# Kernel optimization log

Measured on AMD Instinct MI355X. Metric: run time of the kernel, lower is better.

## Reference

```python
import jax, jax.numpy as jnp
import numpy as np

K, NP, LAT = 400000, 8, 128
# Dense layer dims: (n_p+2) -> 128 -> 128 -> 128 -> 128 -> n_p -> n_p -> (n_p+2)
DIMS = [NP + 2, LAT, LAT, LAT, LAT, NP, NP, NP + 2]


def setup_inputs() -> dict:
    key = jax.random.key(0)
    ks = jax.random.split(key, 8)
    inp = {
        "data": jax.random.normal(ks[0], (K * NP,), dtype=jnp.float32),
        # element node ids: index * (n_p + 1), as assumed by updateElement
        "elements": jnp.arange(K, dtype=jnp.int32) * (NP + 1),
    }
    for i in range(7):
        inp[f"W{i}"] = jax.random.normal(ks[i + 1], (DIMS[i], DIMS[i + 1]), dtype=jnp.float32) / np.float32(np.sqrt(DIMS[i]))
        inp[f"b{i}"] = jnp.zeros((DIMS[i + 1],), dtype=jnp.float32)
    return inp


def _forward(data, elements, Ws, bs):
    k = elements.shape[0]
    n_p = data.size // k
    d2 = data.reshape(k, n_p)                      # (k, n_p)
    e = elements // (n_p + 1)                      # element indices 0..k-1
    left = (e - 1) % k                             # periodic left neighbor
    right = (e + 1) % k                            # periodic right neighbor
    # gather: [left elem last node, own n_p nodes, right elem first node]
    sent = jnp.concatenate(
        [d2[left, -1][:, None], d2[e], d2[right, 0][:, None]], axis=1
    )                                              # (k, n_p+2)
    # ResNetBlock: for each block size: Dense -> relu -> Dense; then final Dense; residual add
    f = sent
    for i in range(0, 6, 2):
        f = jax.nn.relu(f @ Ws[i] + bs[i])
        f = f @ Ws[i + 1] + bs[i + 1]
    f = f @ Ws[6] + bs[6]                          # (k, n_p+2)
    out = sent + f
    return out[:, 1:-1].reshape(-1)                # drop halo cols, flatten to (k*n_p,)


def reference(data, elements, W0, b0, W1, b1, W2, b2, W3, b3, W4, b4, W5, b5, W6, b6):
    Ws = [W0, W1, W2, W3, W4, W5, W6]
    bs = [b0, b1, b2, b3, b4, b5, b6]
    return _forward(data, elements, Ws, bs)
```

## Files before the change

kernel.cpp:

```cpp
#include <hip/hip_runtime.h>
#include <stdint.h>

#define KTOT 400000

typedef __attribute__((ext_vector_type(8))) short sh8;
typedef __attribute__((ext_vector_type(4))) float f32x4;

typedef sh8      __attribute__((may_alias)) sh8_a;
typedef uint64_t __attribute__((may_alias)) u64_a;
typedef uint4    __attribute__((may_alias)) uint4_a;
typedef float4   __attribute__((may_alias)) float4_a;

__device__ __forceinline__ ushort f2bf(float f){
  union { float f; uint32_t u; } v; v.f = f;
  return (ushort)((v.u + 0x7FFFu + ((v.u >> 16) & 1u)) >> 16);
}

__device__ __forceinline__ int actoff(int rt, int bi, int kbyte){
  return (((rt << 4) + bi) << 8) + (kbyte ^ ((bi & 7) << 4));
}

template<int KS, int NT, bool RELU>
__device__ __forceinline__ void layerf(const uint4* __restrict__ wf,
                                       const float* __restrict__ bp,
                                       char* actb, int lane)
{
  const int bi = lane & 15, g = lane >> 4;
  sh8 w[KS][NT];
  #pragma unroll
  for (int ks = 0; ks < KS; ks++)
    #pragma unroll
    for (int nt = 0; nt < NT; nt++)
      w[ks][nt] = __builtin_bit_cast(sh8, wf[(ks*NT + nt)*64 + lane]);

  float4 bv[NT];
  #pragma unroll
  for (int nt = 0; nt < NT; nt++)
    bv[nt] = *(const float4_a*)(bp + nt*16 + g*4);

  #pragma unroll
  for (int rt = 0; rt < 4; rt++){
    sh8 a[KS];
    #pragma unroll
    for (int ks = 0; ks < KS; ks++)
      a[ks] = *(const sh8_a*)(actb + actoff(rt, bi, ks*64 + g*16));

    f32x4 acc[NT];
    #pragma unroll
    for (int nt = 0; nt < NT; nt++)
      acc[nt] = (f32x4){bv[nt].x, bv[nt].y, bv[nt].z, bv[nt].w};

    #pragma unroll
    for (int ks = 0; ks < KS; ks++)
      #pragma unroll
      for (int nt = 0; nt < NT; nt++)
        acc[nt] = __builtin_amdgcn_mfma_f32_16x16x32_bf16(w[ks][nt], a[ks], acc[nt], 0, 0, 0);

    #pragma unroll
    for (int nt = 0; nt < NT; nt++){
      float x0 = acc[nt][0], x1 = acc[nt][1], x2 = acc[nt][2], x3 = acc[nt][3];
      if (RELU){ x0 = fmaxf(x0, 0.f); x1 = fmaxf(x1, 0.f);
                 x2 = fmaxf(x2, 0.f); x3 = fmaxf(x3, 0.f); }
      uint32_t lo = (uint32_t)f2bf(x0) | ((uint32_t)f2bf(x1) << 16);
      uint32_t hi = (uint32_t)f2bf(x2) | ((uint32_t)f2bf(x3) << 16);
      uint64_t pk = (uint64_t)lo | ((uint64_t)hi << 32);
      *(u64_a*)(actb + actoff(rt, bi, nt*32 + g*8)) = pk;
    }
  }
  __syncthreads();
}

__global__ __launch_bounds__(64, 2)
void gnn_kernel(const float* __restrict__ data, const int* __restrict__ elements,
                const uint4* __restrict__ wf, const float* __restrict__ bp,
                float* __restrict__ out)
{
  __shared__ uint4 actsm[1024];
  __shared__ __align__(16) float fbuf[256];
  char* actb = (char*)actsm;
  const int lane = threadIdx.x;
  const int r0 = blockIdx.x * 64;

  #pragma unroll
  for (int rt = 0; rt < 4; rt++){
    if (lane < 16){
      int row = r0 + (rt << 4) + lane;
      int e = elements[row] / 9;
      int le = (e == 0) ? KTOT - 1 : e - 1;
      int re = (e == KTOT - 1) ? 0 : e + 1;
      float lf = data[le*8 + 7];
      float4 d0 = *(const float4_a*)(data + e*8);
      float4 d1 = *(const float4_a*)(data + e*8 + 4);
      float rf = data[re*8];
      ushort s0=f2bf(lf),  s1=f2bf(d0.x), s2=f2bf(d0.y), s3=f2bf(d0.z), s4=f2bf(d0.w),
             s5=f2bf(d1.x), s6=f2bf(d1.y), s7=f2bf(d1.z), s8=f2bf(d1.w), s9=f2bf(rf);
      uint32_t p0 = s0 | ((uint32_t)s1 << 16), p1 = s2 | ((uint32_t)s3 << 16),
               p2 = s4 | ((uint32_t)s5 << 16), p3 = s6 | ((uint32_t)s7 << 16),
               p4 = s8 | ((uint32_t)s9 << 16);
      *(uint4_a*)(actb + actoff(rt, lane, 0 )) = make_uint4(p0, p1, p2, p3);
      *(uint4_a*)(actb + actoff(rt, lane, 16)) = make_uint4(p4, 0, 0, 0);
      *(uint4_a*)(actb + actoff(rt, lane, 32)) = make_uint4(0, 0, 0, 0);
      *(uint4_a*)(actb + actoff(rt, lane, 48)) = make_uint4(0, 0, 0, 0);
    }
  }
  __syncthreads();

  layerf<1, 8, true >(wf +   0*64, bp +   0, actb, lane);
  layerf<4, 8, false>(wf +   8*64, bp + 128, actb, lane);
  layerf<4, 8, true >(wf +  40*64, bp + 256, actb, lane);
  layerf<4, 8, false>(wf +  72*64, bp + 384, actb, lane);
  layerf<4, 1, true >(wf + 104*64, bp + 512, actb, lane);
  layerf<1, 1, false>(wf + 108*64, bp + 528, actb, lane);

  {
    const int bi = lane & 15, g = lane >> 4;
    sh8 w = __builtin_bit_cast(sh8, wf[109*64 + lane]);
    float4 bv = *(const float4_a*)(bp + 544 + g*4);
    #pragma unroll
    for (int rt = 0; rt < 4; rt++){
      sh8 a = *(const sh8_a*)(actb + actoff(rt, bi, g*16));
      f32x4 acc = (f32x4){bv.x, bv.y, bv.z, bv.w};
      acc = __builtin_amdgcn_mfma_f32_16x16x32_bf16(w, a, acc, 0, 0, 0);
      *(float4_a*)(&fbuf[bi*16 + g*4]) = make_float4(acc[0], acc[1], acc[2], acc[3]);
      __syncthreads();
      #pragma unroll
      for (int t = 0; t < 2; t++){
        int i = lane + t*64;
        int rr = i >> 3, c = i & 7;
        int row = r0 + (rt << 4) + rr;
        int e = elements[row] / 9;
        out[row*8 + c] = data[e*8 + c] + fbuf[rr*16 + c + 1];
      }
      __syncthreads();
    }
  }
}

__global__ void prep_kernel(const float* __restrict__ W0, const float* __restrict__ b0,
                            const float* __restrict__ W1, const float* __restrict__ b1,
                            const float* __restrict__ W2, const float* __restrict__ b2,
                            const float* __restrict__ W3, const float* __restrict__ b3,
                            const float* __restrict__ W4, const float* __restrict__ b4,
                            const float* __restrict__ W5, const float* __restrict__ b5,
                            const float* __restrict__ W6, const float* __restrict__ b6,
                            uint4* __restrict__ wsfrag, float* __restrict__ biaspad)
{
  int tid = blockIdx.x * 256 + threadIdx.x;
  if (tid < 110*64){
    int frag = tid >> 6, lane = tid & 63;
    const int off[8] = {0, 8, 40, 72, 104, 108, 109, 110};
    const int Kd[7]  = {10, 128, 128, 128, 128, 8, 8};
    const int Nd[7]  = {128, 128, 128, 128, 8, 8, 10};
    const int NTt[7] = {8, 8, 8, 8, 1, 1, 1};
    int l = 0;
    while (frag >= off[l+1]) l++;
    int local = frag - off[l];
    int nt = local % NTt[l];
    int ks = local / NTt[l];
    const float* W = (l==0)?W0:(l==1)?W1:(l==2)?W2:(l==3)?W3:(l==4)?W4:(l==5)?W5:W6;
    int K = Kd[l], N = Nd[l];
    int n = nt*16 + (lane & 15);
    int kbase = ks*32 + ((lane >> 4) << 3);
    ushort us[8];
    #pragma unroll
    for (int j = 0; j < 8; j++){
      int k = kbase + j;
      float v = (k < K && n < N) ? W[k*N + n] : 0.f;
      us[j] = f2bf(v);
    }
    uint32_t p0 = (uint32_t)us[0] | ((uint32_t)us[1] << 16);
    uint32_t p1 = (uint32_t)us[2] | ((uint32_t)us[3] << 16);
    uint32_t p2 = (uint32_t)us[4] | ((uint32_t)us[5] << 16);
    uint32_t p3 = (uint32_t)us[6] | ((uint32_t)us[7] << 16);
    wsfrag[frag*64 + lane] = make_uint4(p0, p1, p2, p3);
  } else if (tid < 110*64 + 560){
    int i = tid - 110*64;
    float v;
    if (i < 512){
      int l = i >> 7, idx = i & 127;
      const float* B = (l==0)?b0:(l==1)?b1:(l==2)?b2:b3;
      v = B[idx];
    } else {
      int j = i - 512;
      int l = j >> 4, idx = j & 15;
      const float* B = (l==0)?b4:(l==1)?b5:b6;
      int N = (l==2) ? 10 : 8;
      v = (idx < N) ? B[idx] : 0.f;
    }
    biaspad[i] = v;
  }
}

extern "C" void kernel_launch(void* const* d_in, const int* in_sizes, int n_in,
                              void* d_out, int out_size, void* d_ws, size_t ws_size,
                              hipStream_t stream)
{
  const float* data     = (const float*)d_in[0];
  const int*   elements = (const int*)  d_in[1];
  const float* W[7]; const float* B[7];
  for (int i = 0; i < 7; i++){ W[i] = (const float*)d_in[2 + 2*i]; B[i] = (const float*)d_in[3 + 2*i]; }

  uint4* wf = (uint4*)d_ws;
  float* bp = (float*)((char*)d_ws + 110*64*16);

  prep_kernel<<<30, 256, 0, stream>>>(W[0],B[0],W[1],B[1],W[2],B[2],W[3],B[3],
                                      W[4],B[4],W[5],B[5],W[6],B[6], wf, bp);
  gnn_kernel<<<KTOT/64, 64, 0, stream>>>(data, elements, wf, bp, (float*)d_out);
}
```

Before: 154.9 us.

## Fold the last two linear layers into one and parallelize the input gather

The final two dense layers have no activation between them, so W5·W6 and b5·W6+b6 are premultiplied in the prep kernel, removing one MFMA layer and one barrier from the main kernel. A zero pad is written after layer 4's outputs so the folded layer's K=32 MFMA reads zeros. The input gather now uses all 64 lanes, one row each, instead of 16 lanes looping over four row tiles. bf16 conversion switches to the HIP intrinsic. Folding changes rounding slightly because the intermediate bf16 step is gone.

```diff
diff --git a/kernel.cpp b/kernel.cpp
--- a/kernel.cpp
+++ b/kernel.cpp
@@ -1,4 +1,5 @@
 #include <hip/hip_runtime.h>
+#include <hip/hip_bf16.h>
 #include <stdint.h>
 
 #define KTOT 400000
@@ -7,20 +8,22 @@
 typedef __attribute__((ext_vector_type(4))) float f32x4;
 
 typedef sh8      __attribute__((may_alias)) sh8_a;
-typedef uint64_t __attribute__((may_alias)) u64_a;
+typedef uint2    __attribute__((may_alias)) uint2_a;
 typedef uint4    __attribute__((may_alias)) uint4_a;
 typedef float4   __attribute__((may_alias)) float4_a;
 
-__device__ __forceinline__ ushort f2bf(float f){
-  union { float f; uint32_t u; } v; v.f = f;
-  return (ushort)((v.u + 0x7FFFu + ((v.u >> 16) & 1u)) >> 16);
+__device__ __forceinline__ ushort f2bf16(float f){
+  return __builtin_bit_cast(ushort, __float2bfloat16(f));
+}
+__device__ __forceinline__ uint32_t pkbf(float lo, float hi){
+  return (uint32_t)f2bf16(lo) | ((uint32_t)f2bf16(hi) << 16);
 }
 
 __device__ __forceinline__ int actoff(int rt, int bi, int kbyte){
   return (((rt << 4) + bi) << 8) + (kbyte ^ ((bi & 7) << 4));
 }
 
-template<int KS, int NT, bool RELU>
+template<int KS, int NT, bool RELU, bool ZPAD>
 __device__ __forceinline__ void layerf(const uint4* __restrict__ wf,
                                        const float* __restrict__ bp,
                                        char* actb, int lane)
@@ -61,11 +64,11 @@
       float x0 = acc[nt][0], x1 = acc[nt][1], x2 = acc[nt][2], x3 = acc[nt][3];
       if (RELU){ x0 = fmaxf(x0, 0.f); x1 = fmaxf(x1, 0.f);
                  x2 = fmaxf(x2, 0.f); x3 = fmaxf(x3, 0.f); }
-      uint32_t lo = (uint32_t)f2bf(x0) | ((uint32_t)f2bf(x1) << 16);
-      uint32_t hi = (uint32_t)f2bf(x2) | ((uint32_t)f2bf(x3) << 16);
-      uint64_t pk = (uint64_t)lo | ((uint64_t)hi << 32);
-      *(u64_a*)(actb + actoff(rt, bi, nt*32 + g*8)) = pk;
-    }
+      uint32_t lo = pkbf(x0, x1), hi = pkbf(x2, x3);
+      *(uint2_a*)(actb + actoff(rt, bi, nt*32 + g*8)) = make_uint2(lo, hi);
+    }
+    if (ZPAD)
+      *(uint2_a*)(actb + actoff(rt, bi, 32 + g*8)) = make_uint2(0u, 0u);
   }
   __syncthreads();
 }
@@ -80,42 +83,36 @@
   char* actb = (char*)actsm;
   const int lane = threadIdx.x;
   const int r0 = blockIdx.x * 64;
-
-  #pragma unroll
-  for (int rt = 0; rt < 4; rt++){
-    if (lane < 16){
-      int row = r0 + (rt << 4) + lane;
-      int e = elements[row] / 9;
-      int le = (e == 0) ? KTOT - 1 : e - 1;
-      int re = (e == KTOT - 1) ? 0 : e + 1;
-      float lf = data[le*8 + 7];
-      float4 d0 = *(const float4_a*)(data + e*8);
-      float4 d1 = *(const float4_a*)(data + e*8 + 4);
-      float rf = data[re*8];
-      ushort s0=f2bf(lf),  s1=f2bf(d0.x), s2=f2bf(d0.y), s3=f2bf(d0.z), s4=f2bf(d0.w),
-             s5=f2bf(d1.x), s6=f2bf(d1.y), s7=f2bf(d1.z), s8=f2bf(d1.w), s9=f2bf(rf);
-      uint32_t p0 = s0 | ((uint32_t)s1 << 16), p1 = s2 | ((uint32_t)s3 << 16),
-               p2 = s4 | ((uint32_t)s5 << 16), p3 = s6 | ((uint32_t)s7 << 16),
-               p4 = s8 | ((uint32_t)s9 << 16);
-      *(uint4_a*)(actb + actoff(rt, lane, 0 )) = make_uint4(p0, p1, p2, p3);
-      *(uint4_a*)(actb + actoff(rt, lane, 16)) = make_uint4(p4, 0, 0, 0);
-      *(uint4_a*)(actb + actoff(rt, lane, 32)) = make_uint4(0, 0, 0, 0);
-      *(uint4_a*)(actb + actoff(rt, lane, 48)) = make_uint4(0, 0, 0, 0);
-    }
+  const int bi = lane & 15, g = lane >> 4;
+
+  {
+    int row = r0 + lane;
+    int e = elements[row] / 9;
+    int le = (e == 0) ? KTOT - 1 : e - 1;
+    int re = (e == KTOT - 1) ? 0 : e + 1;
+    float lf = data[le*8 + 7];
+    float4 d0 = *(const float4_a*)(data + e*8);
+    float4 d1 = *(const float4_a*)(data + e*8 + 4);
+    float rf = data[re*8];
+    uint32_t p0 = pkbf(lf,   d0.x), p1 = pkbf(d0.y, d0.z),
+             p2 = pkbf(d0.w, d1.x), p3 = pkbf(d1.y, d1.z),
+             p4 = pkbf(d1.w, rf);
+    *(uint4_a*)(actb + actoff(g, bi, 0 )) = make_uint4(p0, p1, p2, p3);
+    *(uint4_a*)(actb + actoff(g, bi, 16)) = make_uint4(p4, 0, 0, 0);
+    *(uint4_a*)(actb + actoff(g, bi, 32)) = make_uint4(0, 0, 0, 0);
+    *(uint4_a*)(actb + actoff(g, bi, 48)) = make_uint4(0, 0, 0, 0);
   }
   __syncthreads();
 
-  layerf<1, 8, true >(wf +   0*64, bp +   0, actb, lane);
-  layerf<4, 8, false>(wf +   8*64, bp + 128, actb, lane);
-  layerf<4, 8, true >(wf +  40*64, bp + 256, actb, lane);
-  layerf<4, 8, false>(wf +  72*64, bp + 384, actb, lane);
-  layerf<4, 1, true >(wf + 104*64, bp + 512, actb, lane);
-  layerf<1, 1, false>(wf + 108*64, bp + 528, actb, lane);
+  layerf<1, 8, true , false>(wf +   0*64, bp +   0, actb, lane);
+  layerf<4, 8, false, false>(wf +   8*64, bp + 128, actb, lane);
+  layerf<4, 8, true , false>(wf +  40*64, bp + 256, actb, lane);
+  layerf<4, 8, false, false>(wf +  72*64, bp + 384, actb, lane);
+  layerf<4, 1, true , true >(wf + 104*64, bp + 512, actb, lane);
 
   {
-    const int bi = lane & 15, g = lane >> 4;
-    sh8 w = __builtin_bit_cast(sh8, wf[109*64 + lane]);
-    float4 bv = *(const float4_a*)(bp + 544 + g*4);
+    sh8 w = __builtin_bit_cast(sh8, wf[108*64 + lane]);
+    float4 bv = *(const float4_a*)(bp + 528 + g*4);
     #pragma unroll
     for (int rt = 0; rt < 4; rt++){
       sh8 a = *(const sh8_a*)(actb + actoff(rt, bi, g*16));
@@ -146,18 +143,18 @@
                             uint4* __restrict__ wsfrag, float* __restrict__ biaspad)
 {
   int tid = blockIdx.x * 256 + threadIdx.x;
-  if (tid < 110*64){
+  if (tid < 109*64){
     int frag = tid >> 6, lane = tid & 63;
-    const int off[8] = {0, 8, 40, 72, 104, 108, 109, 110};
-    const int Kd[7]  = {10, 128, 128, 128, 128, 8, 8};
-    const int Nd[7]  = {128, 128, 128, 128, 8, 8, 10};
-    const int NTt[7] = {8, 8, 8, 8, 1, 1, 1};
+    const int off[7] = {0, 8, 40, 72, 104, 108, 109};
+    const int Kd[6]  = {10, 128, 128, 128, 128, 8};
+    const int Nd[6]  = {128, 128, 128, 128, 8, 10};
+    const int NTt[6] = {8, 8, 8, 8, 1, 1};
     int l = 0;
     while (frag >= off[l+1]) l++;
     int local = frag - off[l];
     int nt = local % NTt[l];
     int ks = local / NTt[l];
-    const float* W = (l==0)?W0:(l==1)?W1:(l==2)?W2:(l==3)?W3:(l==4)?W4:(l==5)?W5:W6;
+    const float* W = (l==0)?W0:(l==1)?W1:(l==2)?W2:(l==3)?W3:W4;
     int K = Kd[l], N = Nd[l];
     int n = nt*16 + (lane & 15);
     int kbase = ks*32 + ((lane >> 4) << 3);
@@ -165,27 +162,43 @@
     #pragma unroll
     for (int j = 0; j < 8; j++){
       int k = kbase + j;
-      float v = (k < K && n < N) ? W[k*N + n] : 0.f;
-      us[j] = f2bf(v);
+      float v = 0.f;
+      if (l == 5){
+        if (k < 8 && n < 10){
+          float s = 0.f;
+          #pragma unroll
+          for (int m = 0; m < 8; m++) s += W5[k*8 + m] * W6[m*10 + n];
+          v = s;
+        }
+      } else if (k < K && n < N){
+        v = W[k*N + n];
+      }
+      us[j] = f2bf16(v);
     }
     uint32_t p0 = (uint32_t)us[0] | ((uint32_t)us[1] << 16);
     uint32_t p1 = (uint32_t)us[2] | ((uint32_t)us[3] << 16);
     uint32_t p2 = (uint32_t)us[4] | ((uint32_t)us[5] << 16);
     uint32_t p3 = (uint32_t)us[6] | ((uint32_t)us[7] << 16);
     wsfrag[frag*64 + lane] = make_uint4(p0, p1, p2, p3);
-  } else if (tid < 110*64 + 560){
-    int i = tid - 110*64;
+  } else if (tid < 109*64 + 544){
+    int i = tid - 109*64;
     float v;
     if (i < 512){
       int l = i >> 7, idx = i & 127;
       const float* B = (l==0)?b0:(l==1)?b1:(l==2)?b2:b3;
       v = B[idx];
+    } else if (i < 528){
+      int idx = i - 512;
+      v = (idx < 8) ? b4[idx] : 0.f;
     } else {
-      int j = i - 512;
-      int l = j >> 4, idx = j & 15;
-      const float* B = (l==0)?b4:(l==1)?b5:b6;
-      int N = (l==2) ? 10 : 8;
-      v = (idx < N) ? B[idx] : 0.f;
+      int n = i - 528;
+      v = 0.f;
+      if (n < 10){
+        float s = b6[n];
+        #pragma unroll
+        for (int m = 0; m < 8; m++) s += b5[m] * W6[m*10 + n];
+        v = s;
+      }
     }
     biaspad[i] = v;
   }
@@ -201,7 +214,7 @@
   for (int i = 0; i < 7; i++){ W[i] = (const float*)d_in[2 + 2*i]; B[i] = (const float*)d_in[3 + 2*i]; }
 
   uint4* wf = (uint4*)d_ws;
-  float* bp = (float*)((char*)d_ws + 110*64*16);
+  float* bp = (float*)((char*)d_ws + 109*64*16);
 
   prep_kernel<<<30, 256, 0, stream>>>(W[0],B[0],W[1],B[1],W[2],B[2],W[3],B[3],
                                       W[4],B[4],W[5],B[5],W[6],B[6], wf, bp);
```

Measured after the change: 149.0 us. -3.8%, faster.
